# Performance work log

Measured on AMD Instinct MI355X. Metric: run time of the kernel, lower is better.

Reference implementation:

```python
import jax, jax.numpy as jnp
import numpy as np

N, E, IN, OUT, R, B = 20000, 640000, 128, 128, 65, 65
BN_EPS = 1e-5


def setup_inputs() -> dict:
    key = jax.random.key(0)
    ks = jax.random.split(key, 8)
    node_feats = jax.random.normal(ks[0], (N, IN), dtype=jnp.float32)
    src = jax.random.randint(ks[1], (E,), 0, N, dtype=jnp.int32)
    dst = jax.random.randint(ks[2], (E,), 0, N, dtype=jnp.int32)
    etype = jax.random.randint(ks[3], (E,), 0, R, dtype=jnp.int32)
    norm = jax.random.uniform(ks[4], (E, 1), dtype=jnp.float32)
    basis = jax.random.normal(ks[5], (B, IN, OUT), dtype=jnp.float32) * 0.05
    comp = jax.random.normal(ks[6], (R, B), dtype=jnp.float32) * 0.1
    h_bias = jnp.zeros((OUT,), dtype=jnp.float32)
    W_res = jax.random.normal(ks[7], (IN, OUT), dtype=jnp.float32) * 0.05
    b_res = jnp.zeros((OUT,), dtype=jnp.float32)
    gamma = jnp.ones((OUT,), dtype=jnp.float32)
    beta = jnp.zeros((OUT,), dtype=jnp.float32)
    return dict(node_feats=node_feats, src=src, dst=dst, etype=etype, norm=norm,
                basis=basis, comp=comp, h_bias=h_bias, W_res=W_res, b_res=b_res,
                gamma=gamma, beta=beta)


def reference(node_feats, src, dst, etype, norm, basis, comp, h_bias, W_res, b_res, gamma, beta):
    n, in_f = node_feats.shape
    r = comp.shape[0]
    # Basis decomposition: W_r = sum_b comp[r,b] * basis[b]  -> (R, in, out)
    W = jnp.einsum('rb,bio->rio', comp, basis)
    # Per-edge message x[src] * norm (norm is scalar per edge so it commutes
    # with the relation matmul). Aggregate per (dst, relation) first, then do
    # one dense relation-batched GEMM (mathematically identical to DGL's
    # per-edge transform + scatter-add, since everything is linear).
    msg = node_feats[src] * norm                       # (E, in)
    seg = dst.astype(jnp.int32) * r + etype            # combined (dst, rel) key
    S = jax.ops.segment_sum(msg, seg, num_segments=n * r).reshape(n, r, in_f)
    h = jnp.einsum('nri,rio->no', S, W) + h_bias       # (N, out)
    h = jax.nn.relu(h)                                 # conv activation (dropout p=0)
    # Residual branch: relu(Linear(x))
    h = h + jax.nn.relu(node_feats @ W_res + b_res)
    # BatchNorm1d (training mode: batch stats, biased variance)
    mean = jnp.mean(h, axis=0)
    var = jnp.var(h, axis=0)
    h = (h - mean) * jax.lax.rsqrt(var + BN_EPS) * gamma + beta
    return h
```

## Files before the change

kernel.cpp:

```cpp
#include <hip/hip_runtime.h>
#include <hip/hip_bf16.h>


#define N_NODES 20000
#define E_EDGES 640000
#define R_REL   65
#define NG5     40
#define NG128   157
#define NSLOT   (NG5 * R_REL * 4)
#define NKEY5   (NG5 * R_REL)
#define NB_RESID 313
#define MAX_TILES 10240
#define TM      128

typedef __attribute__((ext_vector_type(8))) short bf16x8;
typedef __attribute__((ext_vector_type(4))) float f32x4;
typedef __attribute__((ext_vector_type(4))) unsigned int u32x4;
typedef __attribute__((ext_vector_type(2))) unsigned int u32x2;

__device__ __forceinline__ unsigned short f2bf(float x) {
    union { float f; unsigned int u; } c; c.f = x;
    unsigned int b = c.u + 0x7fffu + ((c.u >> 16) & 1u);
    return (unsigned short)(b >> 16);
}
__device__ __forceinline__ float bf2f_lo(unsigned int u) {
    union { unsigned int u; float f; } c; c.u = u << 16; return c.f;
}
__device__ __forceinline__ float bf2f_hi(unsigned int u) {
    union { unsigned int u; float f; } c; c.u = u & 0xffff0000u; return c.f;
}
__device__ __forceinline__ void async16(const void* g, void* l) {
    __builtin_amdgcn_global_load_lds(
        (const __attribute__((address_space(1))) unsigned int*)g,
        (__attribute__((address_space(3))) unsigned int*)l, 16, 0, 0);
}
__device__ __forceinline__ int unperm(int p) {
    return (p & 64) + ((p & 3) << 4) + ((p >> 2) & 15);
}

__global__ void k_prep1(const float* __restrict__ comp, const float* __restrict__ basis,
                        float* __restrict__ W32, const int* __restrict__ et,
                        const int* __restrict__ dstA, int* __restrict__ gh3,
                        int* __restrict__ gh2, const float* __restrict__ node_feats,
                        unsigned short* __restrict__ node_bf) {
    __shared__ int shbuf[15200];
    int b = blockIdx.x, t = threadIdx.x;
    if (b < 320) {
        float* lc = (float*)shbuf;
        int r0 = (b >> 6) * 16;
        int col = (b & 63) * 256 + t;
        for (int j = t; j < 16 * 65; j += 256) {
            int rr = r0 + j / 65;
            lc[j] = (rr < R_REL) ? comp[rr * 65 + (j % 65)] : 0.f;
        }
        __syncthreads();
        float acc[16];
#pragma unroll
        for (int j = 0; j < 16; ++j) acc[j] = 0.f;
        for (int k = 0; k < 65; ++k) {
            float v = basis[k * 16384 + col];
#pragma unroll
            for (int j = 0; j < 16; ++j) acc[j] += lc[j * 65 + k] * v;
        }
#pragma unroll
        for (int j = 0; j < 16; ++j) {
            int rr = r0 + j;
            if (rr < R_REL) W32[rr * 16384 + col] = acc[j];
        }
    } else if (b < 384) {
        int* pk2 = shbuf;
        int* pk3 = shbuf + 10000;
        for (int i = t; i < 15200; i += 256) shbuf[i] = 0;
        __syncthreads();
        for (int i = (b - 320) * 256 + t; i < E_EDGES; i += 64 * 256) {
            int d = dstA[i];
            int slot = ((d >> 9) * 65 + et[i]) * 4 + ((d >> 7) & 3);
            atomicAdd(&pk2[d >> 1], (int)(1u << ((d & 1) << 4)));
            atomicAdd(&pk3[slot >> 1], (int)(1u << ((slot & 1) << 4)));
        }
        __syncthreads();
        for (int i = t; i < 10000; i += 256) {
            unsigned v = (unsigned)pk2[i];
            if (v & 0xffffu) atomicAdd(&gh2[2 * i], (int)(v & 0xffffu));
            if (v >> 16)     atomicAdd(&gh2[2 * i + 1], (int)(v >> 16));
        }
        for (int i = t; i < 5200; i += 256) {
            unsigned v = (unsigned)pk3[i];
            if (v & 0xffffu) atomicAdd(&gh3[2 * i], (int)(v & 0xffffu));
            if (v >> 16)     atomicAdd(&gh3[2 * i + 1], (int)(v >> 16));
        }
    } else {
        int i = (b - 384) * 256 + t;
        if (i < N_NODES * 32) {
            float4 v = reinterpret_cast<const float4*>(node_feats)[i];
            __hip_bfloat162 b0 = __float22bfloat162_rn(make_float2(v.x, v.y));
            __hip_bfloat162 b1 = __float22bfloat162_rn(make_float2(v.z, v.w));
            u32x2 pk;
            pk.x = *reinterpret_cast<unsigned int*>(&b0);
            pk.y = *reinterpret_cast<unsigned int*>(&b1);
            reinterpret_cast<u32x2*>(node_bf)[i] = pk;
        }
    }
}

__global__ void k_prep3(const int* __restrict__ gh3, int* __restrict__ segAll,
                        const int* __restrict__ gh2, int* __restrict__ seg,
                        const float* __restrict__ W32, unsigned short* __restrict__ Wt,
                        const float* __restrict__ Wresf, unsigned short* __restrict__ Wrest) {
    int b = blockIdx.x, t = threadIdx.x;
    if (b < 41) {
        __shared__ int red[256];
        __shared__ int pref;
        int acc = 0;
        for (int i = t; i < b * 256; i += 256) acc += gh3[i];
        red[t] = acc;
        __syncthreads();
        for (int off = 128; off > 0; off >>= 1) {
            if (t < off) red[t] += red[t + off];
            __syncthreads();
        }
        if (t == 0) pref = red[0];
        __syncthreads();
        int i = b * 256 + t;
        int v = (i < NSLOT) ? gh3[i] : 0;
        red[t] = v;
        __syncthreads();
        for (int off = 1; off < 256; off <<= 1) {
            int x = (t >= off) ? red[t - off] : 0;
            __syncthreads();
            red[t] += x;
            __syncthreads();
        }
        int excl = red[t] - v + pref;
        if (i < NSLOT) {
            segAll[i] = excl;
            if (i == NSLOT - 1) segAll[NSLOT] = excl + v;
        }
    } else if (b < 120) {
        __shared__ int red[256];
        __shared__ int pref;
        int b2 = b - 41;
        int acc = 0;
        for (int i = t; i < b2 * 256; i += 256) acc += gh2[i];
        red[t] = acc;
        __syncthreads();
        for (int off = 128; off > 0; off >>= 1) {
            if (t < off) red[t] += red[t + off];
            __syncthreads();
        }
        if (t == 0) pref = red[0];
        __syncthreads();
        int i = b2 * 256 + t;
        int v = (i < N_NODES) ? gh2[i] : 0;
        red[t] = v;
        __syncthreads();
        for (int off = 1; off < 256; off <<= 1) {
            int x = (t >= off) ? red[t - off] : 0;
            __syncthreads();
            red[t] += x;
            __syncthreads();
        }
        int excl = red[t] - v + pref;
        if (i < N_NODES) {
            seg[i] = excl;
            if (i == N_NODES - 1) seg[N_NODES] = excl + v;
        }
    } else {
        __shared__ float tile[64][65];
        int bb = b - 120;
        const float* s; unsigned short* d; int sub;
        if (bb < R_REL * 4) { s = W32 + (size_t)(bb >> 2) * 16384; d = Wt + (size_t)(bb >> 2) * 16384; sub = bb & 3; }
        else { s = Wresf; d = Wrest; sub = bb - R_REL * 4; }
        int ot = (sub >> 1) & 1, itl = sub & 1;
        int tx = t & 63, ty = t >> 6;
        for (int it = 0; it < 16; ++it) {
            int i = ty + it * 4;
            tile[i][tx] = s[(itl * 64 + i) * 128 + ot * 64 + tx];
        }
        __syncthreads();
        for (int it = 0; it < 16; ++it) {
            int o = ty + it * 4;
            d[(ot * 64 + o) * 128 + itl * 64 + tx] = f2bf(tile[tx][o]);
        }
    }
}

__global__ void k_scatterA(const int* __restrict__ et, const int* __restrict__ srcA,
                           const int* __restrict__ dstA, const float* __restrict__ norm,
                           const int* __restrict__ seg, int* __restrict__ cntA,
                           u32x2* __restrict__ ebuf) {
    __shared__ int lh[NG128], lbase[NG128];
    int c0 = blockIdx.x * 2560;
    int cend = min(c0 + 2560, E_EDGES);
    int t = threadIdx.x;
    for (int i = t; i < NG128; i += 256) lh[i] = 0;
    __syncthreads();
    for (int i = c0 + t; i < cend; i += 256) atomicAdd(&lh[dstA[i] >> 7], 1);
    __syncthreads();
    for (int i = t; i < NG128; i += 256)
        if (lh[i] > 0) lbase[i] = seg[i * 128] + atomicAdd(&cntA[i], lh[i]);
    __syncthreads();
    for (int i = t; i < NG128; i += 256) lh[i] = 0;
    __syncthreads();
    for (int i = c0 + t; i < cend; i += 256) {
        int d = dstA[i];
        int g = d >> 7;
        int p = lbase[g] + atomicAdd(&lh[g], 1);
        u32x2 e;
        e.x = (unsigned)srcA[i] | ((unsigned)(d & 127) << 15) | ((unsigned)et[i] << 22);
        e.y = __float_as_uint(norm[i]);
        ebuf[p] = e;
    }
}

__global__ void k_scatterB(const u32x2* __restrict__ ebuf, const int* __restrict__ seg,
                           const int* __restrict__ segAll, int* __restrict__ srcp,
                           float* __restrict__ normp, int* __restrict__ eidx,
                           int* __restrict__ ntiles_p, int* __restrict__ tile_r,
                           int* __restrict__ tile_start, int* __restrict__ tile_len) {
    int b = blockIdx.x, t = threadIdx.x;
    if (b < NG128) {
        __shared__ int base65[R_REL], lcnt[R_REL], sdst[128], ldst[128];
        int g5 = b >> 2, sub = b & 3;
        if (t < R_REL) { base65[t] = segAll[(g5 * 65 + t) * 4 + sub]; lcnt[t] = 0; }
        if (t < 128) {
            int d = b * 128 + t;
            sdst[t] = seg[min(d, N_NODES)];
            ldst[t] = 0;
        }
        __syncthreads();
        int e0 = seg[b * 128];
        int e1 = seg[min((b + 1) * 128, N_NODES)];
        for (int i = e0 + t; i < e1; i += 1024) {
            u32x2 e = ebuf[i];
            int src = e.x & 0x7fff;
            int slot = (e.x >> 15) & 127;
            int rel = e.x >> 22;
            int p = base65[rel] + atomicAdd(&lcnt[rel], 1);
            srcp[p] = src;
            normp[p] = __uint_as_float(e.y);
            int pos = sdst[slot] + atomicAdd(&ldst[slot], 1);
            eidx[pos] = p;
        }
    } else {
        int k2 = (b - NG128) * 1024 + t;
        if (k2 < NKEY5) {
            int s = segAll[k2 * 4], e = segAll[k2 * 4 + 4];
            int len = e - s;
            if (len > 0) {
                int nt = (len + TM - 1) / TM;
                int base = atomicAdd(ntiles_p, nt);
                for (int k = 0; k < nt; ++k) {
                    tile_r[base + k] = k2 % 65;
                    tile_start[base + k] = s + k * TM;
                    tile_len[base + k] = min(TM, len - k * TM);
                }
            }
        }
    }
}

__global__ __launch_bounds__(256, 2) void k_conv_gemm(
    const int* __restrict__ tile_r, const int* __restrict__ tile_start,
    const int* __restrict__ tile_len, const int* __restrict__ ntiles_p,
    const int* __restrict__ srcp, const float* __restrict__ normp,
    const unsigned short* __restrict__ node_bf,
    const unsigned short* __restrict__ Wt, const unsigned short* __restrict__ Wrest,
    const float* __restrict__ b_res, unsigned short* __restrict__ t_out,
    float* __restrict__ resid) {
    __shared__ unsigned short Alds[128 * 128];
    __shared__ unsigned short Blds[128 * 128];
    __shared__ float snorm[128];
    int t = threadIdx.x;
    int w = t >> 6, lane = t & 63;
    int lrow = lane & 15, quad = lane >> 4;

    if (blockIdx.x < NB_RESID) {
        int wr = (w >> 1) * 32, wc = (w & 1) * 64;
        int row0 = blockIdx.x * 64;
        int nrows = min(64, N_NODES - row0);
#pragma unroll
        for (int it = 0; it < 8; ++it) {
            int j = t + 256 * it;
            int o = j >> 4, c = j & 15, cs = c ^ (o & 15);
            async16(Wrest + o * 128 + cs * 8, &Blds[o * 128 + c * 8]);
        }
#pragma unroll
        for (int it = 0; it < 4; ++it) {
            int j = t + 256 * it;
            int p = j >> 4, c = j & 15, cs = c ^ (p & 15);
            if (p < nrows)
                async16(node_bf + (size_t)(row0 + p) * 128 + cs * 8,
                        &Alds[p * 128 + c * 8]);
        }
        __syncthreads();
        f32x4 acc[2][4];
#pragma unroll
        for (int i = 0; i < 2; ++i)
#pragma unroll
            for (int j = 0; j < 4; ++j) acc[i][j] = (f32x4){0.f, 0.f, 0.f, 0.f};
#pragma unroll
        for (int ks = 0; ks < 4; ++ks) {
            int cs = (ks * 4 + quad) ^ lrow;
            bf16x8 af[2], bfr[4];
#pragma unroll
            for (int i = 0; i < 2; ++i)
                af[i] = *reinterpret_cast<const bf16x8*>(&Alds[(wr + i * 16 + lrow) * 128 + cs * 8]);
#pragma unroll
            for (int j = 0; j < 4; ++j)
                bfr[j] = *reinterpret_cast<const bf16x8*>(&Blds[(wc + j * 16 + lrow) * 128 + cs * 8]);
#pragma unroll
            for (int i = 0; i < 2; ++i)
#pragma unroll
                for (int j = 0; j < 4; ++j)
                    acc[i][j] = __builtin_amdgcn_mfma_f32_16x16x32_bf16(af[i], bfr[j], acc[i][j], 0, 0, 0);
        }
        float br0 = b_res[wc + lrow];
        float br1 = b_res[wc + 16 + lrow];
        float br2 = b_res[wc + 32 + lrow];
        float br3 = b_res[wc + 48 + lrow];
#pragma unroll
        for (int i = 0; i < 2; ++i) {
#pragma unroll
            for (int reg = 0; reg < 4; ++reg) {
                int grow = row0 + wr + i * 16 + quad * 4 + reg;
                if (grow < N_NODES) {
                    float4 v;
                    v.x = fmaxf(acc[i][0][reg] + br0, 0.f);
                    v.y = fmaxf(acc[i][1][reg] + br1, 0.f);
                    v.z = fmaxf(acc[i][2][reg] + br2, 0.f);
                    v.w = fmaxf(acc[i][3][reg] + br3, 0.f);
                    *reinterpret_cast<float4*>(resid + (size_t)grow * 128 + wc + lrow * 4) = v;
                }
            }
        }
        return;
    }

    int tid = blockIdx.x - NB_RESID;
    if (tid >= *ntiles_p) return;
    int r = tile_r[tid], start = tile_start[tid], len = tile_len[tid];
    int wr = w * 32;
    const unsigned short* Wr = Wt + (size_t)r * 16384;
#pragma unroll
    for (int it = 0; it < 8; ++it) {
        int j = t + 256 * it;
        int o = j >> 4, c = j & 15, cs = c ^ (o & 15);
        async16(Wr + o * 128 + cs * 8, &Blds[o * 128 + c * 8]);
    }
#pragma unroll
    for (int it = 0; it < 8; ++it) {
        int j = t + 256 * it;
        int p = j >> 4, c = j & 15, cs = c ^ (p & 15);
        if (p < len)
            async16(node_bf + (size_t)srcp[start + p] * 128 + cs * 8,
                    &Alds[p * 128 + c * 8]);
    }
    if (t < TM && t < len) snorm[t] = normp[start + t];
    __syncthreads();

    f32x4 acc[2][8];
#pragma unroll
    for (int i = 0; i < 2; ++i)
#pragma unroll
        for (int j = 0; j < 8; ++j) acc[i][j] = (f32x4){0.f, 0.f, 0.f, 0.f};
#pragma unroll
    for (int ks = 0; ks < 4; ++ks) {
        int cs = (ks * 4 + quad) ^ lrow;
        bf16x8 af[2], bfr[8];
#pragma unroll
        for (int i = 0; i < 2; ++i)
            af[i] = *reinterpret_cast<const bf16x8*>(&Alds[(wr + i * 16 + lrow) * 128 + cs * 8]);
#pragma unroll
        for (int j = 0; j < 8; ++j)
            bfr[j] = *reinterpret_cast<const bf16x8*>(&Blds[(j * 16 + lrow) * 128 + cs * 8]);
#pragma unroll
        for (int i = 0; i < 2; ++i)
#pragma unroll
            for (int j = 0; j < 8; ++j)
                acc[i][j] = __builtin_amdgcn_mfma_f32_16x16x32_bf16(af[i], bfr[j], acc[i][j], 0, 0, 0);
    }

#pragma unroll
    for (int i = 0; i < 2; ++i) {
        int m0 = wr + i * 16 + quad * 4;
#pragma unroll
        for (int reg = 0; reg < 4; ++reg) {
            int m = m0 + reg;
            if (m < len) {
                float nm = snorm[m];
                float2 l0 = make_float2(acc[i][0][reg] * nm, acc[i][1][reg] * nm);
                float2 l1 = make_float2(acc[i][2][reg] * nm, acc[i][3][reg] * nm);
                float2 h0 = make_float2(acc[i][4][reg] * nm, acc[i][5][reg] * nm);
                float2 h1 = make_float2(acc[i][6][reg] * nm, acc[i][7][reg] * nm);
                __hip_bfloat162 bl0 = __float22bfloat162_rn(l0);
                __hip_bfloat162 bl1 = __float22bfloat162_rn(l1);
                __hip_bfloat162 bh0 = __float22bfloat162_rn(h0);
                __hip_bfloat162 bh1 = __float22bfloat162_rn(h1);
                u32x2 s0, s1;
                s0.x = *reinterpret_cast<unsigned int*>(&bl0);
                s0.y = *reinterpret_cast<unsigned int*>(&bl1);
                s1.x = *reinterpret_cast<unsigned int*>(&bh0);
                s1.y = *reinterpret_cast<unsigned int*>(&bh1);
                unsigned short* rowp = t_out + (size_t)(start + m) * 128;
                __builtin_nontemporal_store(s0, reinterpret_cast<u32x2*>(rowp + lrow * 4));
                __builtin_nontemporal_store(s1, reinterpret_cast<u32x2*>(rowp + 64 + lrow * 4));
            }
        }
    }
}

__global__ __launch_bounds__(256) void k_reduce_fused(
    const unsigned short* __restrict__ t, const int* __restrict__ seg,
    const int* __restrict__ eidx, const float* __restrict__ resid,
    const float* __restrict__ h_bias, float* __restrict__ h,
    float* __restrict__ colsum, float* __restrict__ colsumsq) {
    __shared__ float cs1[128], cs2[128], sbias[128];
    if (threadIdx.x < 128) {
        cs1[threadIdx.x] = 0.f; cs2[threadIdx.x] = 0.f;
        sbias[threadIdx.x] = h_bias[unperm(threadIdx.x)];
    }
    __syncthreads();
    int w = threadIdx.x >> 6, lane = threadIdx.x & 63;
    int g = lane >> 4, c = lane & 15;
    for (int k = 0; k < 8; ++k) {
        int d = blockIdx.x * 32 + k * 4 + w;
        if (d >= N_NODES) continue;
        int a = seg[d], b = seg[d + 1];
        float s[8];
#pragma unroll
        for (int kk = 0; kk < 8; ++kk) s[kk] = 0.f;
        for (int q = a + g; q < b; q += 32) {
            int er[8];
#pragma unroll
            for (int kk = 0; kk < 8; ++kk) {
                int row = q + 4 * kk;
                er[kk] = eidx[(row < b) ? row : a];
            }
            u32x4 v[8];
#pragma unroll
            for (int kk = 0; kk < 8; ++kk) {
                v[kk] = *reinterpret_cast<const u32x4*>(t + (size_t)er[kk] * 128 + c * 8);
                if (q + 4 * kk >= b) v[kk] = (u32x4){0u, 0u, 0u, 0u};
            }
#pragma unroll
            for (int kk = 0; kk < 8; ++kk)
#pragma unroll
                for (int j = 0; j < 4; ++j) {
                    s[2 * j]     += bf2f_lo(v[kk][j]);
                    s[2 * j + 1] += bf2f_hi(v[kk][j]);
                }
        }
#pragma unroll
        for (int kk = 0; kk < 8; ++kk) {
            s[kk] += __shfl_xor(s[kk], 16);
            s[kk] += __shfl_xor(s[kk], 32);
        }
        if (g == 0) {
            const float* rp = resid + (size_t)d * 128 + c * 8;
            float4 r0 = *reinterpret_cast<const float4*>(rp);
            float4 r1 = *reinterpret_cast<const float4*>(rp + 4);
            float rr[8] = {r0.x, r0.y, r0.z, r0.w, r1.x, r1.y, r1.z, r1.w};
            float v[8];
#pragma unroll
            for (int kk = 0; kk < 8; ++kk)
                v[kk] = fmaxf(s[kk] + sbias[c * 8 + kk], 0.f) + rr[kk];
            float* hp = h + (size_t)d * 128 + c * 8;
            *reinterpret_cast<float4*>(hp)     = make_float4(v[0], v[1], v[2], v[3]);
            *reinterpret_cast<float4*>(hp + 4) = make_float4(v[4], v[5], v[6], v[7]);
#pragma unroll
            for (int kk = 0; kk < 8; ++kk) {
                atomicAdd(&cs1[c * 8 + kk], v[kk]);
                atomicAdd(&cs2[c * 8 + kk], v[kk] * v[kk]);
            }
        }
    }
    __syncthreads();
    if (threadIdx.x < 128) {
        atomicAdd(&colsum[threadIdx.x], cs1[threadIdx.x]);
        atomicAdd(&colsumsq[threadIdx.x], cs2[threadIdx.x]);
    }
}

__global__ void k_bn(float* __restrict__ h, const float* __restrict__ colsum,
                     const float* __restrict__ colsumsq, const float* __restrict__ gamma,
                     const float* __restrict__ beta) {
    __shared__ float sc[128], sh[128], tile[8][128];
    int t = threadIdx.x;
    if (t < 128) {
        int n = unperm(t);
        float m = colsum[t] * (1.f / N_NODES);
        float var = colsumsq[t] * (1.f / N_NODES) - m * m;
        float s = gamma[n] * rsqrtf(var + 1e-5f);
        sc[t] = s;
        sh[t] = beta[n] - m * s;
    }
    __syncthreads();
    int r = t >> 5;
    int p0 = (t & 31) * 4;
    int n0 = (p0 & 64) + ((p0 >> 2) & 15);
    for (int row0 = blockIdx.x * 8; row0 < N_NODES; row0 += gridDim.x * 8) {
        int row = row0 + r;
        float4 v = make_float4(0.f, 0.f, 0.f, 0.f);
        if (row < N_NODES) v = *reinterpret_cast<float4*>(h + (size_t)row * 128 + p0);
        v.x = v.x * sc[p0] + sh[p0];
        v.y = v.y * sc[p0 + 1] + sh[p0 + 1];
        v.z = v.z * sc[p0 + 2] + sh[p0 + 2];
        v.w = v.w * sc[p0 + 3] + sh[p0 + 3];
        tile[r][n0]      = v.x;
        tile[r][n0 + 16] = v.y;
        tile[r][n0 + 32] = v.z;
        tile[r][n0 + 48] = v.w;
        __syncthreads();
        if (row < N_NODES)
            *reinterpret_cast<float4*>(h + (size_t)row * 128 + p0) =
                *reinterpret_cast<float4*>(&tile[r][p0]);
        __syncthreads();
    }
}

extern "C" void kernel_launch(void* const* d_in, const int* in_sizes, int n_in,
                              void* d_out, int out_size, void* d_ws, size_t ws_size,
                              hipStream_t stream) {
    (void)in_sizes; (void)n_in; (void)out_size; (void)ws_size;
    const float* node_feats = (const float*)d_in[0];
    const int* src    = (const int*)d_in[1];
    const int* dst    = (const int*)d_in[2];
    const int* etype  = (const int*)d_in[3];
    const float* norm = (const float*)d_in[4];
    const float* basis = (const float*)d_in[5];
    const float* comp  = (const float*)d_in[6];
    const float* h_bias = (const float*)d_in[7];
    const float* W_res  = (const float*)d_in[8];
    const float* b_res  = (const float*)d_in[9];
    const float* gamma  = (const float*)d_in[10];
    const float* beta   = (const float*)d_in[11];

    char* ws = (char*)d_ws;
    float* colsum   = (float*)(ws + 0);
    float* colsumsq = (float*)(ws + 512);
    int* ntiles_p   = (int*)(ws + 1024);
    int* cntA       = (int*)(ws + 1088);
    int* gh3        = (int*)(ws + 1792);
    int* gh2        = (int*)(ws + 43392);
    int* segAll     = (int*)(ws + 123392);
    int* seg        = (int*)(ws + 165056);
    int* tile_r     = (int*)(ws + 245120);
    int* tile_start = (int*)(ws + 286080);
    int* tile_len   = (int*)(ws + 327040);
    unsigned short* Wt      = (unsigned short*)(ws + 368000);
    unsigned short* Wrest   = (unsigned short*)(ws + 2497920);
    unsigned short* node_bf = (unsigned short*)(ws + 2530688);
    int* srcp       = (int*)(ws + 7650688);
    float* normp    = (float*)(ws + 10210688);
    int* eidx       = (int*)(ws + 12770688);
    u32x2* ebuf     = (u32x2*)(ws + 15330688);
    float* resid    = (float*)(ws + 20450688);
    const long T_BASE = 30690688L;
    float* W32      = (float*)(ws + T_BASE);
    unsigned short* t_buf = (unsigned short*)(ws + T_BASE);
    float* hacc = (float*)d_out;

    hipMemsetAsync(ws, 0, 123392, stream);
    k_prep1<<<2884, 256, 0, stream>>>(comp, basis, W32, etype, dst, gh3, gh2,
                                      node_feats, node_bf);
    k_prep3<<<384, 256, 0, stream>>>(gh3, segAll, gh2, seg, W32, Wt, W_res, Wrest);
    k_scatterA<<<250, 256, 0, stream>>>(etype, src, dst, norm, seg, cntA, ebuf);
    k_scatterB<<<160, 1024, 0, stream>>>(ebuf, seg, segAll, srcp, normp, eidx,
                                         ntiles_p, tile_r, tile_start, tile_len);
    k_conv_gemm<<<NB_RESID + MAX_TILES, 256, 0, stream>>>(
        tile_r, tile_start, tile_len, ntiles_p, srcp, normp, node_bf,
        Wt, Wrest, b_res, t_buf, resid);
    k_reduce_fused<<<626, 256, 0, stream>>>(t_buf, seg, eidx, resid,
                                            h_bias, hacc, colsum, colsumsq);
    k_bn<<<2500, 256, 0, stream>>>(hacc, colsum, colsumsq, gamma, beta);
}
```

Baseline: 291.8 us.

## Split conv GEMM and reduction into four node-range chunks for L2 reuse

Tiles are bucketed into four chunks by destination-node range (10 groups of 512 nodes each), and the relation GEMM and the fused reduction now run alternately per chunk. The goal is to keep each chunk's intermediate t buffer resident in cache between producer and consumer, so the nontemporal stores are replaced with normal cached stores. The cost is eight launches instead of two, less parallelism per launch with possible tail effects, and a fixed per-chunk tile capacity (CH_TILES) that could overflow on skewed inputs.

New measurement: 388.8 us. +33.3%, slower.

```diff
diff --git a/kernel.cpp b/kernel.cpp
--- a/kernel.cpp
+++ b/kernel.cpp
@@ -10,7 +10,7 @@
 #define NSLOT   (NG5 * R_REL * 4)
 #define NKEY5   (NG5 * R_REL)
 #define NB_RESID 313
-#define MAX_TILES 10240
+#define CH_TILES 4096
 #define TM      128
 
 typedef __attribute__((ext_vector_type(8))) short bf16x8;
@@ -216,7 +216,7 @@
 __global__ void k_scatterB(const u32x2* __restrict__ ebuf, const int* __restrict__ seg,
                            const int* __restrict__ segAll, int* __restrict__ srcp,
                            float* __restrict__ normp, int* __restrict__ eidx,
-                           int* __restrict__ ntiles_p, int* __restrict__ tile_r,
+                           int* __restrict__ ntiles4, int* __restrict__ tile_r,
                            int* __restrict__ tile_start, int* __restrict__ tile_len) {
     int b = blockIdx.x, t = threadIdx.x;
     if (b < NG128) {
@@ -248,12 +248,14 @@
             int s = segAll[k2 * 4], e = segAll[k2 * 4 + 4];
             int len = e - s;
             if (len > 0) {
+                int c = (k2 / 65) / 10;
                 int nt = (len + TM - 1) / TM;
-                int base = atomicAdd(ntiles_p, nt);
-                for (int k = 0; k < nt; ++k) {
-                    tile_r[base + k] = k2 % 65;
-                    tile_start[base + k] = s + k * TM;
-                    tile_len[base + k] = min(TM, len - k * TM);
+                int base = atomicAdd(&ntiles4[c], nt);
+                for (int kk = 0; kk < nt; ++kk) {
+                    int j = c * CH_TILES + base + kk;
+                    tile_r[j] = k2 % 65;
+                    tile_start[j] = s + kk * TM;
+                    tile_len[j] = min(TM, len - kk * TM);
                 }
             }
         }
@@ -262,12 +264,12 @@
 
 __global__ __launch_bounds__(256, 2) void k_conv_gemm(
     const int* __restrict__ tile_r, const int* __restrict__ tile_start,
-    const int* __restrict__ tile_len, const int* __restrict__ ntiles_p,
+    const int* __restrict__ tile_len, const int* __restrict__ ntiles4,
     const int* __restrict__ srcp, const float* __restrict__ normp,
     const unsigned short* __restrict__ node_bf,
     const unsigned short* __restrict__ Wt, const unsigned short* __restrict__ Wrest,
     const float* __restrict__ b_res, unsigned short* __restrict__ t_out,
-    float* __restrict__ resid) {
+    float* __restrict__ resid, int chunk) {
     __shared__ unsigned short Alds[128 * 128];
     __shared__ unsigned short Blds[128 * 128];
     __shared__ float snorm[128];
@@ -275,71 +277,77 @@
     int w = t >> 6, lane = t & 63;
     int lrow = lane & 15, quad = lane >> 4;
 
-    if (blockIdx.x < NB_RESID) {
-        int wr = (w >> 1) * 32, wc = (w & 1) * 64;
-        int row0 = blockIdx.x * 64;
-        int nrows = min(64, N_NODES - row0);
-#pragma unroll
-        for (int it = 0; it < 8; ++it) {
-            int j = t + 256 * it;
-            int o = j >> 4, c = j & 15, cs = c ^ (o & 15);
-            async16(Wrest + o * 128 + cs * 8, &Blds[o * 128 + c * 8]);
-        }
-#pragma unroll
-        for (int it = 0; it < 4; ++it) {
-            int j = t + 256 * it;
-            int p = j >> 4, c = j & 15, cs = c ^ (p & 15);
-            if (p < nrows)
-                async16(node_bf + (size_t)(row0 + p) * 128 + cs * 8,
-                        &Alds[p * 128 + c * 8]);
-        }
-        __syncthreads();
-        f32x4 acc[2][4];
-#pragma unroll
-        for (int i = 0; i < 2; ++i)
-#pragma unroll
-            for (int j = 0; j < 4; ++j) acc[i][j] = (f32x4){0.f, 0.f, 0.f, 0.f};
-#pragma unroll
-        for (int ks = 0; ks < 4; ++ks) {
-            int cs = (ks * 4 + quad) ^ lrow;
-            bf16x8 af[2], bfr[4];
+    int tid;
+    if (chunk == 0) {
+        if (blockIdx.x < NB_RESID) {
+            int wr = (w >> 1) * 32, wc = (w & 1) * 64;
+            int row0 = blockIdx.x * 64;
+            int nrows = min(64, N_NODES - row0);
+#pragma unroll
+            for (int it = 0; it < 8; ++it) {
+                int j = t + 256 * it;
+                int o = j >> 4, c = j & 15, cs = c ^ (o & 15);
+                async16(Wrest + o * 128 + cs * 8, &Blds[o * 128 + c * 8]);
+            }
+#pragma unroll
+            for (int it = 0; it < 4; ++it) {
+                int j = t + 256 * it;
+                int p = j >> 4, c = j & 15, cs = c ^ (p & 15);
+                if (p < nrows)
+                    async16(node_bf + (size_t)(row0 + p) * 128 + cs * 8,
+                            &Alds[p * 128 + c * 8]);
+            }
+            __syncthreads();
+            f32x4 acc[2][4];
 #pragma unroll
             for (int i = 0; i < 2; ++i)
-                af[i] = *reinterpret_cast<const bf16x8*>(&Alds[(wr + i * 16 + lrow) * 128 + cs * 8]);
-#pragma unroll
-            for (int j = 0; j < 4; ++j)
-                bfr[j] = *reinterpret_cast<const bf16x8*>(&Blds[(wc + j * 16 + lrow) * 128 + cs * 8]);
-#pragma unroll
-            for (int i = 0; i < 2; ++i)
+#pragma unroll
+                for (int j = 0; j < 4; ++j) acc[i][j] = (f32x4){0.f, 0.f, 0.f, 0.f};
+#pragma unroll
+            for (int ks = 0; ks < 4; ++ks) {
+                int cs = (ks * 4 + quad) ^ lrow;
+                bf16x8 af[2], bfr[4];
+#pragma unroll
+                for (int i = 0; i < 2; ++i)
+                    af[i] = *reinterpret_cast<const bf16x8*>(&Alds[(wr + i * 16 + lrow) * 128 + cs * 8]);
 #pragma unroll
                 for (int j = 0; j < 4; ++j)
-                    acc[i][j] = __builtin_amdgcn_mfma_f32_16x16x32_bf16(af[i], bfr[j], acc[i][j], 0, 0, 0);
-        }
-        float br0 = b_res[wc + lrow];
-        float br1 = b_res[wc + 16 + lrow];
-        float br2 = b_res[wc + 32 + lrow];
-        float br3 = b_res[wc + 48 + lrow];
-#pragma unroll
-        for (int i = 0; i < 2; ++i) {
-#pragma unroll
-            for (int reg = 0; reg < 4; ++reg) {
-                int grow = row0 + wr + i * 16 + quad * 4 + reg;
-                if (grow < N_NODES) {
-                    float4 v;
-                    v.x = fmaxf(acc[i][0][reg] + br0, 0.f);
-                    v.y = fmaxf(acc[i][1][reg] + br1, 0.f);
-                    v.z = fmaxf(acc[i][2][reg] + br2, 0.f);
-                    v.w = fmaxf(acc[i][3][reg] + br3, 0.f);
-                    *reinterpret_cast<float4*>(resid + (size_t)grow * 128 + wc + lrow * 4) = v;
+                    bfr[j] = *reinterpret_cast<const bf16x8*>(&Blds[(wc + j * 16 + lrow) * 128 + cs * 8]);
+#pragma unroll
+                for (int i = 0; i < 2; ++i)
+#pragma unroll
+                    for (int j = 0; j < 4; ++j)
+                        acc[i][j] = __builtin_amdgcn_mfma_f32_16x16x32_bf16(af[i], bfr[j], acc[i][j], 0, 0, 0);
+            }
+            float br0 = b_res[wc + lrow];
+            float br1 = b_res[wc + 16 + lrow];
+            float br2 = b_res[wc + 32 + lrow];
+            float br3 = b_res[wc + 48 + lrow];
+#pragma unroll
+            for (int i = 0; i < 2; ++i) {
+#pragma unroll
+                for (int reg = 0; reg < 4; ++reg) {
+                    int grow = row0 + wr + i * 16 + quad * 4 + reg;
+                    if (grow < N_NODES) {
+                        float4 v;
+                        v.x = fmaxf(acc[i][0][reg] + br0, 0.f);
+                        v.y = fmaxf(acc[i][1][reg] + br1, 0.f);
+                        v.z = fmaxf(acc[i][2][reg] + br2, 0.f);
+                        v.w = fmaxf(acc[i][3][reg] + br3, 0.f);
+                        *reinterpret_cast<float4*>(resid + (size_t)grow * 128 + wc + lrow * 4) = v;
+                    }
                 }
             }
-        }
-        return;
-    }
-
-    int tid = blockIdx.x - NB_RESID;
-    if (tid >= *ntiles_p) return;
-    int r = tile_r[tid], start = tile_start[tid], len = tile_len[tid];
+            return;
+        }
+        tid = blockIdx.x - NB_RESID;
+    } else {
+        tid = blockIdx.x;
+    }
+
+    if (tid >= ntiles4[chunk]) return;
+    int idx = chunk * CH_TILES + tid;
+    int r = tile_r[idx], start = tile_start[idx], len = tile_len[idx];
     int wr = w * 32;
     const unsigned short* Wr = Wt + (size_t)r * 16384;
 #pragma unroll
@@ -403,8 +411,8 @@
                 s1.x = *reinterpret_cast<unsigned int*>(&bh0);
                 s1.y = *reinterpret_cast<unsigned int*>(&bh1);
                 unsigned short* rowp = t_out + (size_t)(start + m) * 128;
-                __builtin_nontemporal_store(s0, reinterpret_cast<u32x2*>(rowp + lrow * 4));
-                __builtin_nontemporal_store(s1, reinterpret_cast<u32x2*>(rowp + 64 + lrow * 4));
+                *reinterpret_cast<u32x2*>(rowp + lrow * 4)      = s0;
+                *reinterpret_cast<u32x2*>(rowp + 64 + lrow * 4) = s1;
             }
         }
     }
@@ -414,7 +422,7 @@
     const unsigned short* __restrict__ t, const int* __restrict__ seg,
     const int* __restrict__ eidx, const float* __restrict__ resid,
     const float* __restrict__ h_bias, float* __restrict__ h,
-    float* __restrict__ colsum, float* __restrict__ colsumsq) {
+    float* __restrict__ colsum, float* __restrict__ colsumsq, int chunk) {
     __shared__ float cs1[128], cs2[128], sbias[128];
     if (threadIdx.x < 128) {
         cs1[threadIdx.x] = 0.f; cs2[threadIdx.x] = 0.f;
@@ -423,8 +431,8 @@
     __syncthreads();
     int w = threadIdx.x >> 6, lane = threadIdx.x & 63;
     int g = lane >> 4, c = lane & 15;
-    for (int k = 0; k < 8; ++k) {
-        int d = blockIdx.x * 32 + k * 4 + w;
+    for (int k = 0; k < 2; ++k) {
+        int d = chunk * 5120 + blockIdx.x * 8 + k * 4 + w;
         if (d >= N_NODES) continue;
         int a = seg[d], b = seg[d + 1];
         float s[8];
@@ -539,24 +547,24 @@
     char* ws = (char*)d_ws;
     float* colsum   = (float*)(ws + 0);
     float* colsumsq = (float*)(ws + 512);
-    int* ntiles_p   = (int*)(ws + 1024);
+    int* ntiles4    = (int*)(ws + 1024);
     int* cntA       = (int*)(ws + 1088);
     int* gh3        = (int*)(ws + 1792);
     int* gh2        = (int*)(ws + 43392);
     int* segAll     = (int*)(ws + 123392);
     int* seg        = (int*)(ws + 165056);
     int* tile_r     = (int*)(ws + 245120);
-    int* tile_start = (int*)(ws + 286080);
-    int* tile_len   = (int*)(ws + 327040);
-    unsigned short* Wt      = (unsigned short*)(ws + 368000);
-    unsigned short* Wrest   = (unsigned short*)(ws + 2497920);
-    unsigned short* node_bf = (unsigned short*)(ws + 2530688);
-    int* srcp       = (int*)(ws + 7650688);
-    float* normp    = (float*)(ws + 10210688);
-    int* eidx       = (int*)(ws + 12770688);
-    u32x2* ebuf     = (u32x2*)(ws + 15330688);
-    float* resid    = (float*)(ws + 20450688);
-    const long T_BASE = 30690688L;
+    int* tile_start = (int*)(ws + 310656);
+    int* tile_len   = (int*)(ws + 376192);
+    unsigned short* Wt      = (unsigned short*)(ws + 441728);
+    unsigned short* Wrest   = (unsigned short*)(ws + 2571648);
+    unsigned short* node_bf = (unsigned short*)(ws + 2604416);
+    int* srcp       = (int*)(ws + 7724416);
+    float* normp    = (float*)(ws + 10284416);
+    int* eidx       = (int*)(ws + 12844416);
+    u32x2* ebuf     = (u32x2*)(ws + 15404416);
+    float* resid    = (float*)(ws + 20524416);
+    const long T_BASE = 30764416L;
     float* W32      = (float*)(ws + T_BASE);
     unsigned short* t_buf = (unsigned short*)(ws + T_BASE);
     float* hacc = (float*)d_out;
@@ -567,11 +575,13 @@
     k_prep3<<<384, 256, 0, stream>>>(gh3, segAll, gh2, seg, W32, Wt, W_res, Wrest);
     k_scatterA<<<250, 256, 0, stream>>>(etype, src, dst, norm, seg, cntA, ebuf);
     k_scatterB<<<160, 1024, 0, stream>>>(ebuf, seg, segAll, srcp, normp, eidx,
-                                         ntiles_p, tile_r, tile_start, tile_len);
-    k_conv_gemm<<<NB_RESID + MAX_TILES, 256, 0, stream>>>(
-        tile_r, tile_start, tile_len, ntiles_p, srcp, normp, node_bf,
-        Wt, Wrest, b_res, t_buf, resid);
-    k_reduce_fused<<<626, 256, 0, stream>>>(t_buf, seg, eidx, resid,
-                                            h_bias, hacc, colsum, colsumsq);
+                                         ntiles4, tile_r, tile_start, tile_len);
+    for (int c = 0; c < 4; ++c) {
+        k_conv_gemm<<<(c == 0 ? NB_RESID : 0) + CH_TILES, 256, 0, stream>>>(
+            tile_r, tile_start, tile_len, ntiles4, srcp, normp, node_bf,
+            Wt, Wrest, b_res, t_buf, resid, c);
+        k_reduce_fused<<<640, 256, 0, stream>>>(t_buf, seg, eidx, resid,
+                                                h_bias, hacc, colsum, colsumsq, c);
+    }
     k_bn<<<2500, 256, 0, stream>>>(hacc, colsum, colsumsq, gamma, beta);
 }
```

## Load GEMM A operand directly into registers and shrink reduce-kernel blocks

Applied to the files above, without the earlier changes.

The conv GEMM kernel now loads each wave's gathered A-operand rows straight from global memory into registers, instead of staging them through a 32KB LDS tile. This halves LDS use per block and raises the launch-bounds occupancy hint from 2 to 3 blocks per CU. The trade-off is that A fragments are held in registers and fetched with less coalesced per-lane loads. Separately, the reduce kernel now handles 8 destination nodes per block instead of 32 and launches 2500 blocks, which spreads the work more evenly but adds more block-level column-sum atomics.

Result: faster. 285.6 us (-2.1%).

```diff
diff --git a/kernel.cpp b/kernel.cpp
--- a/kernel.cpp
+++ b/kernel.cpp
@@ -260,7 +260,7 @@
     }
 }
 
-__global__ __launch_bounds__(256, 2) void k_conv_gemm(
+__global__ __launch_bounds__(256, 3) void k_conv_gemm(
     const int* __restrict__ tile_r, const int* __restrict__ tile_start,
     const int* __restrict__ tile_len, const int* __restrict__ ntiles_p,
     const int* __restrict__ srcp, const float* __restrict__ normp,
@@ -268,7 +268,6 @@
     const unsigned short* __restrict__ Wt, const unsigned short* __restrict__ Wrest,
     const float* __restrict__ b_res, unsigned short* __restrict__ t_out,
     float* __restrict__ resid) {
-    __shared__ unsigned short Alds[128 * 128];
     __shared__ unsigned short Blds[128 * 128];
     __shared__ float snorm[128];
     int t = threadIdx.x;
@@ -279,20 +278,24 @@
         int wr = (w >> 1) * 32, wc = (w & 1) * 64;
         int row0 = blockIdx.x * 64;
         int nrows = min(64, N_NODES - row0);
+        int r0i = wr + lrow, r1i = wr + 16 + lrow;
+        const bf16x8* a0p = reinterpret_cast<const bf16x8*>(
+            node_bf + (size_t)(row0 + ((r0i < nrows) ? r0i : 0)) * 128);
+        const bf16x8* a1p = reinterpret_cast<const bf16x8*>(
+            node_bf + (size_t)(row0 + ((r1i < nrows) ? r1i : 0)) * 128);
+        bf16x8 areg[2][4];
+#pragma unroll
+        for (int ks = 0; ks < 4; ++ks) {
+            int cq = ks * 4 + quad;
+            areg[0][ks] = a0p[cq];
+            areg[1][ks] = a1p[cq];
+        }
 #pragma unroll
         for (int it = 0; it < 8; ++it) {
             int j = t + 256 * it;
             int o = j >> 4, c = j & 15, cs = c ^ (o & 15);
             async16(Wrest + o * 128 + cs * 8, &Blds[o * 128 + c * 8]);
         }
-#pragma unroll
-        for (int it = 0; it < 4; ++it) {
-            int j = t + 256 * it;
-            int p = j >> 4, c = j & 15, cs = c ^ (p & 15);
-            if (p < nrows)
-                async16(node_bf + (size_t)(row0 + p) * 128 + cs * 8,
-                        &Alds[p * 128 + c * 8]);
-        }
         __syncthreads();
         f32x4 acc[2][4];
 #pragma unroll
@@ -302,10 +305,7 @@
 #pragma unroll
         for (int ks = 0; ks < 4; ++ks) {
             int cs = (ks * 4 + quad) ^ lrow;
-            bf16x8 af[2], bfr[4];
-#pragma unroll
-            for (int i = 0; i < 2; ++i)
-                af[i] = *reinterpret_cast<const bf16x8*>(&Alds[(wr + i * 16 + lrow) * 128 + cs * 8]);
+            bf16x8 bfr[4];
 #pragma unroll
             for (int j = 0; j < 4; ++j)
                 bfr[j] = *reinterpret_cast<const bf16x8*>(&Blds[(wc + j * 16 + lrow) * 128 + cs * 8]);
@@ -313,7 +313,7 @@
             for (int i = 0; i < 2; ++i)
 #pragma unroll
                 for (int j = 0; j < 4; ++j)
-                    acc[i][j] = __builtin_amdgcn_mfma_f32_16x16x32_bf16(af[i], bfr[j], acc[i][j], 0, 0, 0);
+                    acc[i][j] = __builtin_amdgcn_mfma_f32_16x16x32_bf16(areg[i][ks], bfr[j], acc[i][j], 0, 0, 0);
         }
         float br0 = b_res[wc + lrow];
         float br1 = b_res[wc + 16 + lrow];
@@ -341,6 +341,18 @@
     if (tid >= *ntiles_p) return;
     int r = tile_r[tid], start = tile_start[tid], len = tile_len[tid];
     int wr = w * 32;
+    int r0i = wr + lrow, r1i = wr + 16 + lrow;
+    int s0 = srcp[start + ((r0i < len) ? r0i : 0)];
+    int s1 = srcp[start + ((r1i < len) ? r1i : 0)];
+    const bf16x8* a0p = reinterpret_cast<const bf16x8*>(node_bf + (size_t)s0 * 128);
+    const bf16x8* a1p = reinterpret_cast<const bf16x8*>(node_bf + (size_t)s1 * 128);
+    bf16x8 areg[2][4];
+#pragma unroll
+    for (int ks = 0; ks < 4; ++ks) {
+        int cq = ks * 4 + quad;
+        areg[0][ks] = a0p[cq];
+        areg[1][ks] = a1p[cq];
+    }
     const unsigned short* Wr = Wt + (size_t)r * 16384;
 #pragma unroll
     for (int it = 0; it < 8; ++it) {
@@ -348,14 +360,6 @@
         int o = j >> 4, c = j & 15, cs = c ^ (o & 15);
         async16(Wr + o * 128 + cs * 8, &Blds[o * 128 + c * 8]);
     }
-#pragma unroll
-    for (int it = 0; it < 8; ++it) {
-        int j = t + 256 * it;
-        int p = j >> 4, c = j & 15, cs = c ^ (p & 15);
-        if (p < len)
-            async16(node_bf + (size_t)srcp[start + p] * 128 + cs * 8,
-                    &Alds[p * 128 + c * 8]);
-    }
     if (t < TM && t < len) snorm[t] = normp[start + t];
     __syncthreads();
 
@@ -367,10 +371,7 @@
 #pragma unroll
     for (int ks = 0; ks < 4; ++ks) {
         int cs = (ks * 4 + quad) ^ lrow;
-        bf16x8 af[2], bfr[8];
-#pragma unroll
-        for (int i = 0; i < 2; ++i)
-            af[i] = *reinterpret_cast<const bf16x8*>(&Alds[(wr + i * 16 + lrow) * 128 + cs * 8]);
+        bf16x8 bfr[8];
 #pragma unroll
         for (int j = 0; j < 8; ++j)
             bfr[j] = *reinterpret_cast<const bf16x8*>(&Blds[(j * 16 + lrow) * 128 + cs * 8]);
@@ -378,7 +379,7 @@
         for (int i = 0; i < 2; ++i)
 #pragma unroll
             for (int j = 0; j < 8; ++j)
-                acc[i][j] = __builtin_amdgcn_mfma_f32_16x16x32_bf16(af[i], bfr[j], acc[i][j], 0, 0, 0);
+                acc[i][j] = __builtin_amdgcn_mfma_f32_16x16x32_bf16(areg[i][ks], bfr[j], acc[i][j], 0, 0, 0);
     }
 
 #pragma unroll
@@ -397,14 +398,14 @@
                 __hip_bfloat162 bl1 = __float22bfloat162_rn(l1);
                 __hip_bfloat162 bh0 = __float22bfloat162_rn(h0);
                 __hip_bfloat162 bh1 = __float22bfloat162_rn(h1);
-                u32x2 s0, s1;
-                s0.x = *reinterpret_cast<unsigned int*>(&bl0);
-                s0.y = *reinterpret_cast<unsigned int*>(&bl1);
-                s1.x = *reinterpret_cast<unsigned int*>(&bh0);
-                s1.y = *reinterpret_cast<unsigned int*>(&bh1);
+                u32x2 s0v, s1v;
+                s0v.x = *reinterpret_cast<unsigned int*>(&bl0);
+                s0v.y = *reinterpret_cast<unsigned int*>(&bl1);
+                s1v.x = *reinterpret_cast<unsigned int*>(&bh0);
+                s1v.y = *reinterpret_cast<unsigned int*>(&bh1);
                 unsigned short* rowp = t_out + (size_t)(start + m) * 128;
-                __builtin_nontemporal_store(s0, reinterpret_cast<u32x2*>(rowp + lrow * 4));
-                __builtin_nontemporal_store(s1, reinterpret_cast<u32x2*>(rowp + 64 + lrow * 4));
+                __builtin_nontemporal_store(s0v, reinterpret_cast<u32x2*>(rowp + lrow * 4));
+                __builtin_nontemporal_store(s1v, reinterpret_cast<u32x2*>(rowp + 64 + lrow * 4));
             }
         }
     }
@@ -423,8 +424,8 @@
     __syncthreads();
     int w = threadIdx.x >> 6, lane = threadIdx.x & 63;
     int g = lane >> 4, c = lane & 15;
-    for (int k = 0; k < 8; ++k) {
-        int d = blockIdx.x * 32 + k * 4 + w;
+    for (int k = 0; k < 2; ++k) {
+        int d = blockIdx.x * 8 + k * 4 + w;
         if (d >= N_NODES) continue;
         int a = seg[d], b = seg[d + 1];
         float s[8];
@@ -571,7 +572,7 @@
     k_conv_gemm<<<NB_RESID + MAX_TILES, 256, 0, stream>>>(
         tile_r, tile_start, tile_len, ntiles_p, srcp, normp, node_bf,
         Wt, Wrest, b_res, t_buf, resid);
-    k_reduce_fused<<<626, 256, 0, stream>>>(t_buf, seg, eidx, resid,
-                                            h_bias, hacc, colsum, colsumsq);
+    k_reduce_fused<<<2500, 256, 0, stream>>>(t_buf, seg, eidx, resid,
+                                             h_bias, hacc, colsum, colsumsq);
     k_bn<<<2500, 256, 0, stream>>>(hacc, colsum, colsumsq, gamma, beta);
 }
```
